# Optimization experiments

Measured on AMD Instinct MI355X. Metric: run time of the kernel, lower is better.

## Reference

```python
import jax, jax.numpy as jnp
import numpy as np

N = 50000
E = 400000


def _cheb_norm(edge_index, dtype):
    # PyG ChebConv norm (normalization='sym', lambda_max=2.0):
    # remove self loops, L_hat = -D^{-1/2} A D^{-1/2} on off-diagonal edges.
    src, dst = edge_index[0], edge_index[1]
    mask = (src != dst).astype(dtype)
    deg = jax.ops.segment_sum(mask, src, num_segments=N)
    dinv = jnp.where(deg > 0, jax.lax.rsqrt(jnp.where(deg > 0, deg, 1.0)), 0.0)
    w = -dinv[src] * dinv[dst] * mask  # [E]
    return src, dst, w


def _cheb_conv(x, src, dst, w, W0, W1, b):
    # out = T0(x) W0 + T1(x) W1 + b, T0 = x, T1 = L_hat x
    tx1 = jax.ops.segment_sum(w[:, None] * x[src], dst, num_segments=N)
    return x @ W0 + tx1 @ W1 + b


def setup_inputs() -> dict:
    key = jax.random.key(0)
    ks = jax.random.split(key, 12)
    s = 0.05
    inp = {
        "x": jax.random.normal(ks[0], (N, 128), dtype=jnp.float32),
        "edge_index": jax.random.randint(ks[1], (2, E), 0, N, dtype=jnp.int64),
        "W1_0": jax.random.normal(ks[2], (128, 256), dtype=jnp.float32) * s,
        "W1_1": jax.random.normal(ks[3], (128, 256), dtype=jnp.float32) * s,
        "b1": jnp.zeros((256,), dtype=jnp.float32),
        "W2_0": jax.random.normal(ks[4], (256, 256), dtype=jnp.float32) * s,
        "W2_1": jax.random.normal(ks[5], (256, 256), dtype=jnp.float32) * s,
        "b2": jnp.zeros((256,), dtype=jnp.float32),
        "W3_0": jax.random.normal(ks[6], (256, 256), dtype=jnp.float32) * s,
        "W3_1": jax.random.normal(ks[7], (256, 256), dtype=jnp.float32) * s,
        "b3": jnp.zeros((256,), dtype=jnp.float32),
    }
    return inp


def reference(x, edge_index, W1_0, W1_1, b1, W2_0, W2_1, b2, W3_0, W3_1, b3):
    # Eval mode: F.dropout with training=False is identity, so dropout is omitted.
    src, dst, w = _cheb_norm(edge_index, x.dtype)
    h = jax.nn.relu(_cheb_conv(x, src, dst, w, W1_0, W1_1, b1))
    h = jax.nn.relu(_cheb_conv(h, src, dst, w, W2_0, W2_1, b2))
    h = _cheb_conv(h, src, dst, w, W3_0, W3_1, b3)
    return h
```

## Files before the change

### kernel.cpp

```cpp
#include <hip/hip_runtime.h>
#include <hip/hip_bf16.h>


typedef __attribute__((ext_vector_type(8))) short bf16x8;
typedef __attribute__((ext_vector_type(4))) float f32x4;

__device__ __forceinline__ float bf2f(unsigned int lo16) {
    unsigned int t = lo16 << 16;
    return __builtin_bit_cast(float, t);
}
__device__ __forceinline__ unsigned short f2bf(float f) {
    unsigned int u = __builtin_bit_cast(unsigned int, f);
    unsigned int r = (u + 0x7fffu + ((u >> 16) & 1u)) >> 16;
    return (unsigned short)r;
}

__global__ __launch_bounds__(256) void deg_cnt_kernel(const int* __restrict__ src,
                                                      const int* __restrict__ dst,
                                                      float* __restrict__ deg,
                                                      int* __restrict__ cnt, int E) {
    int e = blockIdx.x * blockDim.x + threadIdx.x;
    if (e < E) {
        int s = src[e], d = dst[e];
        if (s != d) atomicAdd(&deg[s], 1.0f);
        atomicAdd(&cnt[d], 1);
    }
}

__global__ __launch_bounds__(256) void scan_partial_dinv(const int* __restrict__ cnt,
                                                         int* __restrict__ part,
                                                         float* __restrict__ deg, int N) {
    __shared__ int lds[256];
    int tid = threadIdx.x;
    int base = blockIdx.x * 1024 + tid * 4;
    int s = 0;
    #pragma unroll
    for (int i = 0; i < 4; ++i) {
        if (base + i < N) {
            s += cnt[base + i];
            float d = deg[base + i];
            deg[base + i] = (d > 0.0f) ? rsqrtf(d) : 0.0f;
        }
    }
    lds[tid] = s;
    __syncthreads();
    for (int off = 128; off > 0; off >>= 1) {
        if (tid < off) lds[tid] += lds[tid + off];
        __syncthreads();
    }
    if (tid == 0) part[blockIdx.x] = lds[0];
}

__global__ __launch_bounds__(64) void scan_small(int* __restrict__ part, int NB,
                                                 int* __restrict__ rowptr, int N) {
    if (threadIdx.x == 0 && blockIdx.x == 0) {
        int total = 0;
        for (int i = 0; i < NB; ++i) { int t = part[i]; part[i] = total; total += t; }
        rowptr[N] = total;
    }
}

__global__ __launch_bounds__(256) void scan_chunk(const int* __restrict__ cnt,
                                                  const int* __restrict__ part,
                                                  int* __restrict__ rowptr, int N) {
    __shared__ int lds[256];
    int tid = threadIdx.x;
    int base = blockIdx.x * 1024 + tid * 4;
    int c[4];
    #pragma unroll
    for (int i = 0; i < 4; ++i) c[i] = (base + i < N) ? cnt[base + i] : 0;
    int ts = c[0] + c[1] + c[2] + c[3];
    lds[tid] = ts;
    __syncthreads();
    for (int off = 1; off < 256; off <<= 1) {
        int v = (tid >= off) ? lds[tid - off] : 0;
        __syncthreads();
        lds[tid] += v;
        __syncthreads();
    }
    int o = part[blockIdx.x] + lds[tid] - ts;
    #pragma unroll
    for (int i = 0; i < 4; ++i) {
        if (base + i < N) rowptr[base + i] = o;
        o += c[i];
    }
}

__global__ __launch_bounds__(256) void fill_kernel(const int* __restrict__ src,
                                                   const int* __restrict__ dst,
                                                   const float* __restrict__ dinv,
                                                   const int* __restrict__ rowptr,
                                                   int* __restrict__ cnt2,
                                                   int* __restrict__ esrc,
                                                   float* __restrict__ ew, int E) {
    int e = blockIdx.x * blockDim.x + threadIdx.x;
    if (e < E) {
        int s = src[e], d = dst[e];
        int pos = rowptr[d] + atomicAdd(&cnt2[d], 1);
        esrc[pos] = s;
        ew[pos] = (s != d) ? (-dinv[s] * dinv[d]) : 0.0f;
    }
}

__global__ __launch_bounds__(256) void cast_x_kernel(const float* __restrict__ x,
                                                     unsigned short* __restrict__ xb,
                                                     long long n4) {
    long long i = (long long)blockIdx.x * 256 + threadIdx.x;
    if (i >= n4) return;
    float4 v = reinterpret_cast<const float4*>(x)[i];
    ushort4 o;
    o.x = f2bf(v.x); o.y = f2bf(v.y); o.z = f2bf(v.z); o.w = f2bf(v.w);
    reinterpret_cast<ushort4*>(xb)[i] = o;
}

struct TParams {
    const float* W[6];
    unsigned short* WT[6];
    int K[6];
};
__global__ __launch_bounds__(256) void transpose_cast_all(TParams p) {
    int m = blockIdx.z;
    int K = p.K[m];
    int kb = blockIdx.x * 32, nb = blockIdx.y * 32;
    if (kb >= K) return;
    const float* W = p.W[m];
    unsigned short* WT = p.WT[m];
    __shared__ float t[32][33];
    int lx = threadIdx.x & 31, ly = threadIdx.x >> 5;
    #pragma unroll
    for (int i = 0; i < 32; i += 8)
        t[ly + i][lx] = W[(size_t)(kb + ly + i) * 256 + nb + lx];
    __syncthreads();
    #pragma unroll
    for (int i = 0; i < 32; i += 8)
        WT[(size_t)(nb + ly + i) * K + kb + lx] = f2bf(t[lx][ly + i]);
}

template <int V> struct RowT;
template <> struct RowT<2> { using T = unsigned int; };
template <> struct RowT<4> { using T = uint2; };

__device__ __forceinline__ void fma_row(float* acc, unsigned int u, float wv) {
    acc[0] += wv * bf2f(u & 0xffffu);
    acc[1] += wv * bf2f(u >> 16);
}
__device__ __forceinline__ void fma_row(float* acc, uint2 u, float wv) {
    acc[0] += wv * bf2f(u.x & 0xffffu);
    acc[1] += wv * bf2f(u.x >> 16);
    acc[2] += wv * bf2f(u.y & 0xffffu);
    acc[3] += wv * bf2f(u.y >> 16);
}

template <int F>
__global__ __launch_bounds__(256) void gather_bf16(const int* __restrict__ rowptr,
                                                   const int* __restrict__ esrc,
                                                   const float* __restrict__ ew,
                                                   const unsigned short* __restrict__ xb,
                                                   unsigned short* __restrict__ txb,
                                                   int N) {
    constexpr int V = F / 64;
    using T = typename RowT<V>::T;
    int wave = threadIdx.x >> 6, lane = threadIdx.x & 63;
    int n = blockIdx.x * 4 + wave;
    if (n >= N) return;
    int beg = rowptr[n], end = rowptr[n + 1];
    float acc[V] = {};

    int k = beg;
    for (; k + 4 <= end; k += 4) {
        int s0 = esrc[k], s1 = esrc[k + 1], s2 = esrc[k + 2], s3 = esrc[k + 3];
        float w0 = ew[k], w1 = ew[k + 1], w2 = ew[k + 2], w3 = ew[k + 3];
        T r0 = *reinterpret_cast<const T*>(&xb[(size_t)s0 * F + lane * V]);
        T r1 = *reinterpret_cast<const T*>(&xb[(size_t)s1 * F + lane * V]);
        T r2 = *reinterpret_cast<const T*>(&xb[(size_t)s2 * F + lane * V]);
        T r3 = *reinterpret_cast<const T*>(&xb[(size_t)s3 * F + lane * V]);
        fma_row(acc, r0, w0);
        fma_row(acc, r1, w1);
        fma_row(acc, r2, w2);
        fma_row(acc, r3, w3);
    }
    for (; k < end; ++k) {
        int s = esrc[k];
        float wv = ew[k];
        T r = *reinterpret_cast<const T*>(&xb[(size_t)s * F + lane * V]);
        fma_row(acc, r, wv);
    }

    unsigned short* q = &txb[(size_t)n * F + lane * V];
    if (V == 2) {
        unsigned int o = (unsigned int)f2bf(acc[0]) | ((unsigned int)f2bf(acc[1]) << 16);
        *reinterpret_cast<unsigned int*>(q) = o;
    } else {
        uint2 o;
        o.x = (unsigned int)f2bf(acc[0]) | ((unsigned int)f2bf(acc[1]) << 16);
        o.y = (unsigned int)f2bf(acc[2]) | ((unsigned int)f2bf(acc[3]) << 16);
        *reinterpret_cast<uint2*>(q) = o;
    }
}

template <int K, bool RELU, typename OutT>
__global__ __launch_bounds__(256, 3) void gemm_mfma(const unsigned short* __restrict__ Xb,
                                                    const unsigned short* __restrict__ Tb,
                                                    const unsigned short* __restrict__ W0T,
                                                    const unsigned short* __restrict__ W1T,
                                                    const float* __restrict__ bias,
                                                    OutT* __restrict__ out, int M) {
    constexpr int SA = 72;
    __shared__ unsigned short As[64 * SA];
    __shared__ unsigned short Bs[256 * SA];

    const int tid = threadIdx.x;
    const int wave = tid >> 6;
    const int lane = tid & 63;
    const int l15 = lane & 15;
    const int quad = lane >> 4;
    const int row0 = blockIdx.x * 64;

    const int srow = tid >> 3;
    const int scol = (tid & 7) * 8;

    f32x4 acc[4][4];
    #pragma unroll
    for (int i = 0; i < 4; ++i)
        #pragma unroll
        for (int j = 0; j < 4; ++j) acc[i][j] = (f32x4){0.f, 0.f, 0.f, 0.f};

    #pragma unroll
    for (int pass = 0; pass < 2; ++pass) {
        const unsigned short* Amat = pass ? Tb : Xb;
        const unsigned short* Wmat = pass ? W1T : W0T;
        for (int k0 = 0; k0 < K; k0 += 64) {
            if (pass != 0 || k0 != 0) __syncthreads();
            #pragma unroll
            for (int r = 0; r < 2; ++r) {
                int row = r * 32 + srow;
                int grow = row0 + row; if (grow > M - 1) grow = M - 1;
                uint4 v = *reinterpret_cast<const uint4*>(&Amat[(size_t)grow * K + k0 + scol]);
                *reinterpret_cast<uint4*>(&As[row * SA + scol]) = v;
            }
            #pragma unroll
            for (int r = 0; r < 8; ++r) {
                int row = r * 32 + srow;
                uint4 v = *reinterpret_cast<const uint4*>(&Wmat[(size_t)row * K + k0 + scol]);
                *reinterpret_cast<uint4*>(&Bs[row * SA + scol]) = v;
            }
            __syncthreads();

            #pragma unroll
            for (int kf = 0; kf < 2; ++kf) {
                const int koff = kf * 32 + quad * 8;
                bf16x8 a[4], b[4];
                #pragma unroll
                for (int mt = 0; mt < 4; ++mt)
                    a[mt] = *reinterpret_cast<const bf16x8*>(&As[(mt * 16 + l15) * SA + koff]);
                #pragma unroll
                for (int nt = 0; nt < 4; ++nt)
                    b[nt] = *reinterpret_cast<const bf16x8*>(
                        &Bs[(wave * 64 + nt * 16 + l15) * SA + koff]);
                #pragma unroll
                for (int mt = 0; mt < 4; ++mt)
                    #pragma unroll
                    for (int nt = 0; nt < 4; ++nt)
                        acc[mt][nt] = __builtin_amdgcn_mfma_f32_16x16x32_bf16(
                            a[mt], b[nt], acc[mt][nt], 0, 0, 0);
            }
        }
    }

    #pragma unroll
    for (int mt = 0; mt < 4; ++mt) {
        #pragma unroll
        for (int r = 0; r < 4; ++r) {
            int m = row0 + mt * 16 + quad * 4 + r;
            if (m >= M) continue;
            #pragma unroll
            for (int nt = 0; nt < 4; ++nt) {
                int n = wave * 64 + nt * 16 + l15;
                float v = acc[mt][nt][r] + bias[n];
                if (RELU) v = fmaxf(v, 0.0f);
                if constexpr (sizeof(OutT) == 2)
                    out[(size_t)m * 256 + n] = (OutT)f2bf(v);
                else
                    out[(size_t)m * 256 + n] = (OutT)v;
            }
        }
    }
}

static inline size_t align_up(size_t v, size_t a) { return (v + a - 1) / a * a; }

extern "C" void kernel_launch(void* const* d_in, const int* in_sizes, int n_in,
                              void* d_out, int out_size, void* d_ws, size_t ws_size,
                              hipStream_t stream) {
    const float* x    = (const float*)d_in[0];
    const int*   ei   = (const int*)d_in[1];
    const float* W1_0 = (const float*)d_in[2];
    const float* W1_1 = (const float*)d_in[3];
    const float* b1   = (const float*)d_in[4];
    const float* W2_0 = (const float*)d_in[5];
    const float* W2_1 = (const float*)d_in[6];
    const float* b2   = (const float*)d_in[7];
    const float* W3_0 = (const float*)d_in[8];
    const float* W3_1 = (const float*)d_in[9];
    const float* b3   = (const float*)d_in[10];
    float* out = (float*)d_out;

    const int N = in_sizes[0] / 128;
    const int E = in_sizes[1] / 2;
    const int* src = ei;
    const int* dst = ei + E;

    typedef unsigned short u16;
    char* ws = (char*)d_ws;
    size_t off = 0;
    float* dinv   = (float*)(ws + off); off = align_up(off + (size_t)N * 4, 256);
    int*   cnt    = (int*)  (ws + off); off = align_up(off + (size_t)N * 4, 256);
    int*   cnt2   = (int*)  (ws + off); off = align_up(off + (size_t)N * 4, 256);
    size_t zero_end = off;
    int*   rowptr = (int*)  (ws + off); off = align_up(off + (size_t)(N + 1) * 4, 256);
    int*   part   = (int*)  (ws + off); off = align_up(off + 256 * 4, 256);
    int*   esrc   = (int*)  (ws + off); off = align_up(off + (size_t)E * 4, 256);
    float* ew     = (float*)(ws + off); off = align_up(off + (size_t)E * 4, 256);
    u16*   xb     = (u16*)  (ws + off); off = align_up(off + (size_t)N * 128 * 2, 256);
    u16*   txb    = (u16*)  (ws + off); off = align_up(off + (size_t)N * 256 * 2, 256);
    u16*   h1b    = (u16*)  (ws + off); off = align_up(off + (size_t)N * 256 * 2, 256);
    u16*   h2b    = (u16*)  (ws + off); off = align_up(off + (size_t)N * 256 * 2, 256);
    u16*   W10T   = (u16*)  (ws + off); off = align_up(off + (size_t)256 * 128 * 2, 256);
    u16*   W11T   = (u16*)  (ws + off); off = align_up(off + (size_t)256 * 128 * 2, 256);
    u16*   W20T   = (u16*)  (ws + off); off = align_up(off + (size_t)256 * 256 * 2, 256);
    u16*   W21T   = (u16*)  (ws + off); off = align_up(off + (size_t)256 * 256 * 2, 256);
    u16*   W30T   = (u16*)  (ws + off); off = align_up(off + (size_t)256 * 256 * 2, 256);
    u16*   W31T   = (u16*)  (ws + off); off = align_up(off + (size_t)256 * 256 * 2, 256);
    (void)ws_size;

    const int TB = 256;
    dim3 gE((E + TB - 1) / TB);
    const int NB = (N + 1023) / 1024;

    hipMemsetAsync(dinv, 0, zero_end, stream);
    deg_cnt_kernel<<<gE, TB, 0, stream>>>(src, dst, dinv, cnt, E);
    scan_partial_dinv<<<NB, 256, 0, stream>>>(cnt, part, dinv, N);
    scan_small<<<1, 64, 0, stream>>>(part, NB, rowptr, N);
    scan_chunk<<<NB, 256, 0, stream>>>(cnt, part, rowptr, N);
    fill_kernel<<<gE, TB, 0, stream>>>(src, dst, dinv, rowptr, cnt2, esrc, ew, E);

    {
        long long n4 = (long long)N * 128 / 4;
        cast_x_kernel<<<(unsigned)((n4 + 255) / 256), TB, 0, stream>>>(x, xb, n4);
    }
    {
        TParams p;
        p.W[0] = W1_0; p.WT[0] = W10T; p.K[0] = 128;
        p.W[1] = W1_1; p.WT[1] = W11T; p.K[1] = 128;
        p.W[2] = W2_0; p.WT[2] = W20T; p.K[2] = 256;
        p.W[3] = W2_1; p.WT[3] = W21T; p.K[3] = 256;
        p.W[4] = W3_0; p.WT[4] = W30T; p.K[4] = 256;
        p.W[5] = W3_1; p.WT[5] = W31T; p.K[5] = 256;
        transpose_cast_all<<<dim3(8, 8, 6), TB, 0, stream>>>(p);
    }

    dim3 gemmGrid((N + 63) / 64);
    dim3 gatherGrid((N + 3) / 4);

    gather_bf16<128><<<gatherGrid, TB, 0, stream>>>(rowptr, esrc, ew, xb, txb, N);
    gemm_mfma<128, true, u16><<<gemmGrid, TB, 0, stream>>>(xb, txb, W10T, W11T, b1, h1b, N);

    gather_bf16<256><<<gatherGrid, TB, 0, stream>>>(rowptr, esrc, ew, h1b, txb, N);
    gemm_mfma<256, true, u16><<<gemmGrid, TB, 0, stream>>>(h1b, txb, W20T, W21T, b2, h2b, N);

    gather_bf16<256><<<gatherGrid, TB, 0, stream>>>(rowptr, esrc, ew, h2b, txb, N);
    gemm_mfma<256, false, float><<<gemmGrid, TB, 0, stream>>>(h2b, txb, W30T, W31T, b3, out, N);
}
```

Before: 353.4 us.

## Fuse prep kernels, warp-scan partials, half-wave gather, direct-to-LDS swizzled GEMM loads

Merges the degree count, x cast and weight transpose into a single prep launch, and replaces the serial partial-sum scan with a wave shuffle scan. The gather now uses 32 lanes per node with wider 8- or 16-byte row loads. The GEMM stages tiles with global_load_lds into an XOR-swizzled unpadded LDS layout instead of register round trips. Together these aim to cut launch count, serial work and LDS/register staging costs, but the swizzle indexing and the scan's NB<=64 limit must stay consistent.

```diff
diff --git a/kernel.cpp b/kernel.cpp
--- a/kernel.cpp
+++ b/kernel.cpp
@@ -15,16 +15,59 @@
     return (unsigned short)r;
 }
 
-__global__ __launch_bounds__(256) void deg_cnt_kernel(const int* __restrict__ src,
-                                                      const int* __restrict__ dst,
-                                                      float* __restrict__ deg,
-                                                      int* __restrict__ cnt, int E) {
-    int e = blockIdx.x * blockDim.x + threadIdx.x;
-    if (e < E) {
-        int s = src[e], d = dst[e];
-        if (s != d) atomicAdd(&deg[s], 1.0f);
-        atomicAdd(&cnt[d], 1);
-    }
+struct PrepParams {
+    const int* src;
+    const int* dst;
+    float* deg;
+    int* cnt;
+    int E;
+    const float* x;
+    unsigned short* xb;
+    int gE;
+    int gC;
+    const float* W[6];
+    unsigned short* WT[6];
+    int K[6];
+};
+
+__global__ __launch_bounds__(256) void prep_kernel(PrepParams p) {
+    __shared__ float t[32][33];
+    int b = blockIdx.x;
+    int tid = threadIdx.x;
+    if (b < p.gE) {
+        int e = b * 256 + tid;
+        if (e < p.E) {
+            int s = p.src[e], d = p.dst[e];
+            if (s != d) atomicAdd(&p.deg[s], 1.0f);
+            atomicAdd(&p.cnt[d], 1);
+        }
+        return;
+    }
+    b -= p.gE;
+    if (b < p.gC) {
+        long long i = (long long)b * 256 + tid;
+        float4 v = reinterpret_cast<const float4*>(p.x)[i];
+        ushort4 o;
+        o.x = f2bf(v.x); o.y = f2bf(v.y); o.z = f2bf(v.z); o.w = f2bf(v.w);
+        reinterpret_cast<ushort4*>(p.xb)[i] = o;
+        return;
+    }
+    b -= p.gC;
+    int m = b >> 6;
+    int rem = b & 63;
+    int K = p.K[m];
+    int kb = (rem & 7) * 32, nb = (rem >> 3) * 32;
+    if (kb >= K) return;
+    const float* W = p.W[m];
+    unsigned short* WT = p.WT[m];
+    int lx = tid & 31, ly = tid >> 5;
+    #pragma unroll
+    for (int i = 0; i < 32; i += 8)
+        t[ly + i][lx] = W[(size_t)(kb + ly + i) * 256 + nb + lx];
+    __syncthreads();
+    #pragma unroll
+    for (int i = 0; i < 32; i += 8)
+        WT[(size_t)(nb + ly + i) * K + kb + lx] = f2bf(t[lx][ly + i]);
 }
 
 __global__ __launch_bounds__(256) void scan_partial_dinv(const int* __restrict__ cnt,
@@ -53,11 +96,16 @@
 
 __global__ __launch_bounds__(64) void scan_small(int* __restrict__ part, int NB,
                                                  int* __restrict__ rowptr, int N) {
-    if (threadIdx.x == 0 && blockIdx.x == 0) {
-        int total = 0;
-        for (int i = 0; i < NB; ++i) { int t = part[i]; part[i] = total; total += t; }
-        rowptr[N] = total;
-    }
+    int lane = threadIdx.x;
+    int v = (lane < NB) ? part[lane] : 0;
+    int inc = v;
+    #pragma unroll
+    for (int off = 1; off < 64; off <<= 1) {
+        int t = __shfl_up(inc, off, 64);
+        if (lane >= off) inc += t;
+    }
+    if (lane < NB) part[lane] = inc - v;
+    if (lane == 63) rowptr[N] = inc;
 }
 
 __global__ __launch_bounds__(256) void scan_chunk(const int* __restrict__ cnt,
@@ -102,53 +150,39 @@
     }
 }
 
-__global__ __launch_bounds__(256) void cast_x_kernel(const float* __restrict__ x,
-                                                     unsigned short* __restrict__ xb,
-                                                     long long n4) {
-    long long i = (long long)blockIdx.x * 256 + threadIdx.x;
-    if (i >= n4) return;
-    float4 v = reinterpret_cast<const float4*>(x)[i];
-    ushort4 o;
-    o.x = f2bf(v.x); o.y = f2bf(v.y); o.z = f2bf(v.z); o.w = f2bf(v.w);
-    reinterpret_cast<ushort4*>(xb)[i] = o;
-}
-
-struct TParams {
-    const float* W[6];
-    unsigned short* WT[6];
-    int K[6];
-};
-__global__ __launch_bounds__(256) void transpose_cast_all(TParams p) {
-    int m = blockIdx.z;
-    int K = p.K[m];
-    int kb = blockIdx.x * 32, nb = blockIdx.y * 32;
-    if (kb >= K) return;
-    const float* W = p.W[m];
-    unsigned short* WT = p.WT[m];
-    __shared__ float t[32][33];
-    int lx = threadIdx.x & 31, ly = threadIdx.x >> 5;
-    #pragma unroll
-    for (int i = 0; i < 32; i += 8)
-        t[ly + i][lx] = W[(size_t)(kb + ly + i) * 256 + nb + lx];
-    __syncthreads();
-    #pragma unroll
-    for (int i = 0; i < 32; i += 8)
-        WT[(size_t)(nb + ly + i) * K + kb + lx] = f2bf(t[lx][ly + i]);
-}
-
 template <int V> struct RowT;
-template <> struct RowT<2> { using T = unsigned int; };
 template <> struct RowT<4> { using T = uint2; };
-
-__device__ __forceinline__ void fma_row(float* acc, unsigned int u, float wv) {
-    acc[0] += wv * bf2f(u & 0xffffu);
-    acc[1] += wv * bf2f(u >> 16);
-}
+template <> struct RowT<8> { using T = uint4; };
+
 __device__ __forceinline__ void fma_row(float* acc, uint2 u, float wv) {
     acc[0] += wv * bf2f(u.x & 0xffffu);
     acc[1] += wv * bf2f(u.x >> 16);
     acc[2] += wv * bf2f(u.y & 0xffffu);
     acc[3] += wv * bf2f(u.y >> 16);
+}
+__device__ __forceinline__ void fma_row(float* acc, uint4 u, float wv) {
+    acc[0] += wv * bf2f(u.x & 0xffffu);
+    acc[1] += wv * bf2f(u.x >> 16);
+    acc[2] += wv * bf2f(u.y & 0xffffu);
+    acc[3] += wv * bf2f(u.y >> 16);
+    acc[4] += wv * bf2f(u.z & 0xffffu);
+    acc[5] += wv * bf2f(u.z >> 16);
+    acc[6] += wv * bf2f(u.w & 0xffffu);
+    acc[7] += wv * bf2f(u.w >> 16);
+}
+__device__ __forceinline__ void pack_out(unsigned short* q, const float* acc, uint2*) {
+    uint2 o;
+    o.x = (unsigned int)f2bf(acc[0]) | ((unsigned int)f2bf(acc[1]) << 16);
+    o.y = (unsigned int)f2bf(acc[2]) | ((unsigned int)f2bf(acc[3]) << 16);
+    *reinterpret_cast<uint2*>(q) = o;
+}
+__device__ __forceinline__ void pack_out(unsigned short* q, const float* acc, uint4*) {
+    uint4 o;
+    o.x = (unsigned int)f2bf(acc[0]) | ((unsigned int)f2bf(acc[1]) << 16);
+    o.y = (unsigned int)f2bf(acc[2]) | ((unsigned int)f2bf(acc[3]) << 16);
+    o.z = (unsigned int)f2bf(acc[4]) | ((unsigned int)f2bf(acc[5]) << 16);
+    o.w = (unsigned int)f2bf(acc[6]) | ((unsigned int)f2bf(acc[7]) << 16);
+    *reinterpret_cast<uint4*>(q) = o;
 }
 
 template <int F>
@@ -158,10 +192,11 @@
                                                    const unsigned short* __restrict__ xb,
                                                    unsigned short* __restrict__ txb,
                                                    int N) {
-    constexpr int V = F / 64;
+    constexpr int V = F / 32;
     using T = typename RowT<V>::T;
-    int wave = threadIdx.x >> 6, lane = threadIdx.x & 63;
-    int n = blockIdx.x * 4 + wave;
+    int half = threadIdx.x >> 5;
+    int lane = threadIdx.x & 31;
+    int n = blockIdx.x * 8 + half;
     if (n >= N) return;
     int beg = rowptr[n], end = rowptr[n + 1];
     float acc[V] = {};
@@ -186,16 +221,7 @@
         fma_row(acc, r, wv);
     }
 
-    unsigned short* q = &txb[(size_t)n * F + lane * V];
-    if (V == 2) {
-        unsigned int o = (unsigned int)f2bf(acc[0]) | ((unsigned int)f2bf(acc[1]) << 16);
-        *reinterpret_cast<unsigned int*>(q) = o;
-    } else {
-        uint2 o;
-        o.x = (unsigned int)f2bf(acc[0]) | ((unsigned int)f2bf(acc[1]) << 16);
-        o.y = (unsigned int)f2bf(acc[2]) | ((unsigned int)f2bf(acc[3]) << 16);
-        *reinterpret_cast<uint2*>(q) = o;
-    }
+    pack_out(&txb[(size_t)n * F + lane * V], acc, (T*)nullptr);
 }
 
 template <int K, bool RELU, typename OutT>
@@ -205,9 +231,8 @@
                                                     const unsigned short* __restrict__ W1T,
                                                     const float* __restrict__ bias,
                                                     OutT* __restrict__ out, int M) {
-    constexpr int SA = 72;
-    __shared__ unsigned short As[64 * SA];
-    __shared__ unsigned short Bs[256 * SA];
+    __shared__ unsigned short As[64 * 64];
+    __shared__ unsigned short Bs[256 * 64];
 
     const int tid = threadIdx.x;
     const int wave = tid >> 6;
@@ -215,15 +240,16 @@
     const int l15 = lane & 15;
     const int quad = lane >> 4;
     const int row0 = blockIdx.x * 64;
-
-    const int srow = tid >> 3;
-    const int scol = (tid & 7) * 8;
+    const int swz = ((lane & 7) ^ ((lane >> 3) & 7)) * 8;
 
     f32x4 acc[4][4];
     #pragma unroll
     for (int i = 0; i < 4; ++i)
         #pragma unroll
         for (int j = 0; j < 4; ++j) acc[i][j] = (f32x4){0.f, 0.f, 0.f, 0.f};
+
+    typedef const __attribute__((address_space(1))) void gvoid;
+    typedef __attribute__((address_space(3))) void lvoid;
 
     #pragma unroll
     for (int pass = 0; pass < 2; ++pass) {
@@ -233,30 +259,32 @@
             if (pass != 0 || k0 != 0) __syncthreads();
             #pragma unroll
             for (int r = 0; r < 2; ++r) {
-                int row = r * 32 + srow;
-                int grow = row0 + row; if (grow > M - 1) grow = M - 1;
-                uint4 v = *reinterpret_cast<const uint4*>(&Amat[(size_t)grow * K + k0 + scol]);
-                *reinterpret_cast<uint4*>(&As[row * SA + scol]) = v;
+                int grow = row0 + r * 32 + wave * 8 + (lane >> 3);
+                if (grow > M - 1) grow = M - 1;
+                const unsigned short* gp = &Amat[(size_t)grow * K + k0 + swz];
+                __builtin_amdgcn_global_load_lds((gvoid*)gp,
+                    (lvoid*)&As[(r * 32 + wave * 8) * 64], 16, 0, 0);
             }
             #pragma unroll
             for (int r = 0; r < 8; ++r) {
-                int row = r * 32 + srow;
-                uint4 v = *reinterpret_cast<const uint4*>(&Wmat[(size_t)row * K + k0 + scol]);
-                *reinterpret_cast<uint4*>(&Bs[row * SA + scol]) = v;
+                int brow = r * 32 + wave * 8 + (lane >> 3);
+                const unsigned short* gp = &Wmat[(size_t)brow * K + k0 + swz];
+                __builtin_amdgcn_global_load_lds((gvoid*)gp,
+                    (lvoid*)&Bs[(r * 32 + wave * 8) * 64], 16, 0, 0);
             }
             __syncthreads();
 
             #pragma unroll
             for (int kf = 0; kf < 2; ++kf) {
-                const int koff = kf * 32 + quad * 8;
+                const int col = (((kf * 4 + quad) ^ (l15 & 7)) * 8);
                 bf16x8 a[4], b[4];
                 #pragma unroll
                 for (int mt = 0; mt < 4; ++mt)
-                    a[mt] = *reinterpret_cast<const bf16x8*>(&As[(mt * 16 + l15) * SA + koff]);
+                    a[mt] = *reinterpret_cast<const bf16x8*>(&As[(mt * 16 + l15) * 64 + col]);
                 #pragma unroll
                 for (int nt = 0; nt < 4; ++nt)
                     b[nt] = *reinterpret_cast<const bf16x8*>(
-                        &Bs[(wave * 64 + nt * 16 + l15) * SA + koff]);
+                        &Bs[(wave * 64 + nt * 16 + l15) * 64 + col]);
                 #pragma unroll
                 for (int mt = 0; mt < 4; ++mt)
                     #pragma unroll
@@ -334,33 +362,33 @@
     (void)ws_size;
 
     const int TB = 256;
-    dim3 gE((E + TB - 1) / TB);
+    const int gE = (E + TB - 1) / TB;
+    const int gC = (int)(((long long)N * 128 / 4) / 256);
     const int NB = (N + 1023) / 1024;
 
     hipMemsetAsync(dinv, 0, zero_end, stream);
-    deg_cnt_kernel<<<gE, TB, 0, stream>>>(src, dst, dinv, cnt, E);
-    scan_partial_dinv<<<NB, 256, 0, stream>>>(cnt, part, dinv, N);
-    scan_small<<<1, 64, 0, stream>>>(part, NB, rowptr, N);
-    scan_chunk<<<NB, 256, 0, stream>>>(cnt, part, rowptr, N);
-    fill_kernel<<<gE, TB, 0, stream>>>(src, dst, dinv, rowptr, cnt2, esrc, ew, E);
 
     {
-        long long n4 = (long long)N * 128 / 4;
-        cast_x_kernel<<<(unsigned)((n4 + 255) / 256), TB, 0, stream>>>(x, xb, n4);
-    }
-    {
-        TParams p;
+        PrepParams p;
+        p.src = src; p.dst = dst; p.deg = dinv; p.cnt = cnt; p.E = E;
+        p.x = x; p.xb = xb; p.gE = gE; p.gC = gC;
         p.W[0] = W1_0; p.WT[0] = W10T; p.K[0] = 128;
         p.W[1] = W1_1; p.WT[1] = W11T; p.K[1] = 128;
         p.W[2] = W2_0; p.WT[2] = W20T; p.K[2] = 256;
         p.W[3] = W2_1; p.WT[3] = W21T; p.K[3] = 256;
         p.W[4] = W3_0; p.WT[4] = W30T; p.K[4] = 256;
         p.W[5] = W3_1; p.WT[5] = W31T; p.K[5] = 256;
-        transpose_cast_all<<<dim3(8, 8, 6), TB, 0, stream>>>(p);
-    }
+        prep_kernel<<<gE + gC + 384, TB, 0, stream>>>(p);
+    }
+
+    scan_partial_dinv<<<NB, 256, 0, stream>>>(cnt, part, dinv, N);
+    scan_small<<<1, 64, 0, stream>>>(part, NB, rowptr, N);
+    scan_chunk<<<NB, 256, 0, stream>>>(cnt, part, rowptr, N);
+    fill_kernel<<<(E + TB - 1) / TB, TB, 0, stream>>>(src, dst, dinv, rowptr, cnt2,
+                                                      esrc, ew, E);
 
     dim3 gemmGrid((N + 63) / 64);
-    dim3 gatherGrid((N + 3) / 4);
+    dim3 gatherGrid((N + 7) / 8);
 
     gather_bf16<128><<<gatherGrid, TB, 0, stream>>>(rowptr, esrc, ew, xb, txb, N);
     gemm_mfma<128, true, u16><<<gemmGrid, TB, 0, stream>>>(xb, txb, W10T, W11T, b1, h1b, N);
```

Measured after the change: 329.0 us. 1.07x faster.
